# Kernel tuning notes

Hardware: AMD Instinct MI355X
Metric: run time of the kernel (lower is better)

The kernel has to match this reference:

```python
import jax, jax.numpy as jnp
import numpy as np
import math

D_MODEL = 1024
N_HEADS = 16
SEQ = 1024
BATCH = 4


def setup_inputs() -> dict:
    key = jax.random.key(0)
    ks = jax.random.split(key, 13)
    s = 1.0 / math.sqrt(D_MODEL)  # keep logits in a sane range
    return {
        "x": jax.random.normal(ks[0], (BATCH, SEQ, D_MODEL), jnp.float32),
        "Wq": jax.random.normal(ks[1], (D_MODEL, D_MODEL), jnp.float32) * s,
        "bq": jnp.zeros((D_MODEL,), jnp.float32),
        "Wk": jax.random.normal(ks[2], (D_MODEL, D_MODEL), jnp.float32) * s,
        "bk": jnp.zeros((D_MODEL,), jnp.float32),
        "Wv": jax.random.normal(ks[3], (D_MODEL, D_MODEL), jnp.float32) * s,
        "bv": jnp.zeros((D_MODEL,), jnp.float32),
        "Wo": jax.random.normal(ks[4], (D_MODEL, D_MODEL), jnp.float32) * s,
        "bo": jnp.zeros((D_MODEL,), jnp.float32),
        "Wimp": jax.random.normal(ks[5], (N_HEADS, D_MODEL), jnp.float32) * s,
        "bimp": jnp.zeros((N_HEADS,), jnp.float32),
        "k_ema": jax.random.normal(ks[6], (SEQ, D_MODEL), jnp.float32),
        "v_ema": jax.random.normal(ks[7], (SEQ, D_MODEL), jnp.float32),
    }


def reference(x, Wq, bq, Wk, bk, Wv, bv, Wo, bo, Wimp, bimp, k_ema, v_ema):
    B, S, D = x.shape
    H = Wimp.shape[0]
    hd = D // H

    def proj(W, b):
        # [B,S,D] -> [B,H,S,hd]
        return (x @ W.T + b).reshape(B, S, H, hd).transpose(0, 2, 1, 3)

    q = proj(Wq, bq)
    k = proj(Wk, bk)
    v = proj(Wv, bv)

    scores = jnp.einsum("bhqd,bhkd->bhqk", q, k) / math.sqrt(hd)

    # importance bias: outer-sum of per-head key/value importance vectors
    k_imp = (k_ema[:S] @ Wimp.T + bimp).T  # [H, S]
    v_imp = (v_ema[:S] @ Wimp.T + bimp).T  # [H, S]
    bias = 0.5 * (k_imp[:, :, None] + v_imp[:, None, :])  # [H, S, S]
    scores = scores + 0.1 * bias[None]

    # causal mask (torch masks before bias add; -inf + finite == -inf, so equivalent)
    causal = jnp.triu(jnp.ones((S, S), bool), k=1)
    scores = jnp.where(causal, -jnp.inf, scores)

    attn = jax.nn.softmax(scores, axis=-1)
    out = jnp.einsum("bhqk,bhkd->bhqd", attn, v)
    out = out.transpose(0, 2, 1, 3).reshape(B, S, D)
    return out @ Wo.T + bo
```

## Files before the change

### kernel.cpp

```cpp
#include <hip/hip_runtime.h>
#include <hip/hip_bf16.h>
#include <math.h>

#define D_MODEL 1024
#define SEQ     1024
#define BATCH   4
#define NHEADS  16
#define HD      64

#define QSC 0.18033688f
#define BSC 0.072134752f

typedef __bf16 bf16x8 __attribute__((ext_vector_type(8)));
typedef __bf16 bf16x4 __attribute__((ext_vector_type(4)));
typedef float  f32x4  __attribute__((ext_vector_type(4)));

__device__ __forceinline__ f32x4 mfma16(bf16x8 a, bf16x8 b, f32x4 c) {
  return __builtin_amdgcn_mfma_f32_16x16x32_bf16(a, b, c, 0, 0, 0);
}

__device__ __forceinline__ void async16(__bf16* lds, const __bf16* g) {
  __builtin_amdgcn_global_load_lds(g, lds, 16, 0, 0);
}

__global__ __launch_bounds__(256) void prep_kernel(
    const float* __restrict__ x,
    const float* __restrict__ Wq, const float* __restrict__ Wk,
    const float* __restrict__ Wv, const float* __restrict__ Wo,
    const float* __restrict__ v_ema,
    const float* __restrict__ Wimp, const float* __restrict__ bimp,
    __bf16* __restrict__ x_bf, __bf16* __restrict__ wq_bf, __bf16* __restrict__ wk_bf,
    __bf16* __restrict__ wv_bf, __bf16* __restrict__ wo_bf,
    float* __restrict__ vimp) {
  const int bid = blockIdx.x;
  const int tid = threadIdx.x;
  if (bid < 4096) {
    int i = bid * 256 + tid;
    float4 v = ((const float4*)x)[i];
    bf16x4 o; o[0] = (__bf16)v.x; o[1] = (__bf16)v.y; o[2] = (__bf16)v.z; o[3] = (__bf16)v.w;
    ((bf16x4*)x_bf)[i] = o;
  } else if (bid < 8192) {
    int i = (bid - 4096) * 256 + tid;
    int sel = i >> 18;
    int j = i & 262143;
    const float* s = (sel == 0) ? Wq : (sel == 1) ? Wk : (sel == 2) ? Wv : Wo;
    __bf16* d      = (sel == 0) ? wq_bf : (sel == 1) ? wk_bf : (sel == 2) ? wv_bf : wo_bf;
    float4 v = ((const float4*)s)[j];
    bf16x4 o; o[0] = (__bf16)v.x; o[1] = (__bf16)v.y; o[2] = (__bf16)v.z; o[3] = (__bf16)v.w;
    ((bf16x4*)d)[j] = o;
  } else {
    int gw   = (bid - 8192) * 4 + (tid >> 6);
    int lane = tid & 63;
    int h = gw >> 10, s = gw & 1023;
    float sum = 0.f;
    for (int d = lane; d < D_MODEL; d += 64)
      sum += v_ema[s * D_MODEL + d] * Wimp[h * D_MODEL + d];
    for (int mm = 32; mm >= 1; mm >>= 1) sum += __shfl_xor(sum, mm);
    if (lane == 0) vimp[h * SEQ + s] = sum + bimp[h];
  }
}

template<bool OUT_BF16>
__global__ __launch_bounds__(256) void gemm_bt(
    const __bf16* __restrict__ A,
    const __bf16* __restrict__ W0, const __bf16* __restrict__ W1, const __bf16* __restrict__ W2,
    const float* __restrict__ b0, const float* __restrict__ b1, const float* __restrict__ b2,
    void* out0, void* out1, void* out2, float sc0, float sc1, float sc2) {
  const int z = blockIdx.z;
  const __bf16* W   = (z == 0) ? W0 : (z == 1) ? W1 : W2;
  const float* bias = (z == 0) ? b0 : (z == 1) ? b1 : b2;
  void* out         = (z == 0) ? out0 : (z == 1) ? out1 : out2;
  const float sc    = (z == 0) ? sc0 : (z == 1) ? sc1 : sc2;

  __shared__ __bf16 As[128 * 32];
  __shared__ __bf16 Bs[128 * 32];

  const int tid = threadIdx.x;
  const int w = tid >> 6, l = tid & 63;
  const int quad = l >> 4, l16 = l & 15;
  const int wy = w >> 1, wx = w & 1;
  const int row0 = blockIdx.y * 128;
  const int col0 = blockIdx.x * 128;

  const f32x4 fzero = {0.f, 0.f, 0.f, 0.f};
  f32x4 acc[4][4];
  for (int i = 0; i < 4; i++)
    for (int j = 0; j < 4; j++) acc[i][j] = fzero;

  const int lr = l >> 2;
  const int sw0 = (((l & 3) ^ (lr & 3)) * 8);
  const int rowA = w * 16 + lr;
  const __bf16* aptr = A + (size_t)(row0 + rowA) * D_MODEL + sw0;
  const __bf16* bptr = W + (size_t)(col0 + rowA) * D_MODEL + sw0;
  __bf16* lA0 = &As[w * 512 + l * 8];
  __bf16* lA1 = &As[2048 + w * 512 + l * 8];
  __bf16* lB0 = &Bs[w * 512 + l * 8];
  __bf16* lB1 = &Bs[2048 + w * 512 + l * 8];

  const int rswz = (quad ^ (l16 & 3)) * 8;

  for (int k0 = 0; k0 < D_MODEL; k0 += 32) {
    async16(lA0, aptr + k0);
    async16(lA1, aptr + (size_t)64 * D_MODEL + k0);
    async16(lB0, bptr + k0);
    async16(lB1, bptr + (size_t)64 * D_MODEL + k0);
    __syncthreads();
    bf16x8 af[4], bfr[4];
    #pragma unroll
    for (int mi = 0; mi < 4; mi++) af[mi]  = *(const bf16x8*)&As[(wy * 64 + mi * 16 + l16) * 32 + rswz];
    #pragma unroll
    for (int ni = 0; ni < 4; ni++) bfr[ni] = *(const bf16x8*)&Bs[(wx * 64 + ni * 16 + l16) * 32 + rswz];
    if (z == 1) {
      #pragma unroll
      for (int mi = 0; mi < 4; mi++)
        #pragma unroll
        for (int ni = 0; ni < 4; ni++)
          acc[mi][ni] = mfma16(bfr[ni], af[mi], acc[mi][ni]);
    } else {
      #pragma unroll
      for (int mi = 0; mi < 4; mi++)
        #pragma unroll
        for (int ni = 0; ni < 4; ni++)
          acc[mi][ni] = mfma16(af[mi], bfr[ni], acc[mi][ni]);
    }
    __syncthreads();
  }

  if (z == 1 && OUT_BF16) {
    __bf16* kp = (__bf16*)out;
    #pragma unroll
    for (int ni = 0; ni < 4; ni++) {
      const int wcolbase = col0 + wx * 64 + ni * 16 + quad * 4;
      const float4 b4 = *(const float4*)&bias[wcolbase];
      const float bb[4] = {b4.x, b4.y, b4.z, b4.w};
      #pragma unroll
      for (int mi = 0; mi < 4; mi++) {
        const int token = row0 + wy * 64 + mi * 16 + l16;
        const int bh = (token >> 10) * 16 + (wcolbase >> 6);
        const int colp = ((wcolbase & 63) + ((token & 7) << 3)) & 63;
        union { __bf16 hh[4]; uint2 uu; } pk;
        #pragma unroll
        for (int r = 0; r < 4; r++) pk.hh[r] = (__bf16)(acc[mi][ni][r] + bb[r]);
        *(uint2*)(kp + ((size_t)bh * SEQ + (token & 1023)) * HD + colp) = pk.uu;
      }
    }
  } else if (z == 2 && OUT_BF16) {
    __bf16* vp = (__bf16*)out;
    #pragma unroll
    for (int ni = 0; ni < 4; ni++) {
      const int col = col0 + wx * 64 + ni * 16 + l16;
      const float bv = bias[col];
      #pragma unroll
      for (int mi = 0; mi < 4; mi++) {
        const int token = row0 + wy * 64 + mi * 16 + quad * 4;
        const int bh = (token >> 10) * 16 + (col >> 6);
        const int chk = (token >> 6) & 15;
        const int keyp = ((token & 63) + ((col & 7) << 3)) & 63;
        const size_t base = (((size_t)bh * 16 + chk) * 64 + (col & 63)) * 64 + keyp;
        union { __bf16 hh[4]; uint2 uu; } pk;
        #pragma unroll
        for (int r = 0; r < 4; r++) pk.hh[r] = (__bf16)(acc[mi][ni][r] + bv);
        *(uint2*)(vp + base) = pk.uu;
      }
    }
  } else {
    #pragma unroll
    for (int ni = 0; ni < 4; ni++) {
      const int col = col0 + wx * 64 + ni * 16 + l16;
      const float bv = bias[col];
      #pragma unroll
      for (int mi = 0; mi < 4; mi++) {
        const int row = row0 + wy * 64 + mi * 16 + quad * 4;
        #pragma unroll
        for (int r = 0; r < 4; r++) {
          float v = (acc[mi][ni][r] + bv) * sc;
          if (OUT_BF16) ((__bf16*)out)[(size_t)(row + r) * D_MODEL + col] = (__bf16)v;
          else          ((float*)out)[(size_t)(row + r) * D_MODEL + col] = v;
        }
      }
    }
  }
}

__global__ __launch_bounds__(256, 2) void attn_kernel(
    const __bf16* __restrict__ Qb, const __bf16* __restrict__ Kp,
    const __bf16* __restrict__ Vp, const float* __restrict__ vimp,
    __bf16* __restrict__ Ob) {
  const int id = blockIdx.x;
  const int bh = id & 63;
  const int gg = id >> 6;
  const int b = bh >> 4, h = bh & 15;
  const int tid = threadIdx.x;
  const int wave = tid >> 6, lane = tid & 63;
  const int quad = lane >> 4, l16 = lane & 15;

  __shared__ __bf16 Kl[2][4096];
  __shared__ __bf16 Vl[2][4096];
  __shared__ __bf16 Ps[4][16][72];

  const __bf16* kbase = Kp + (size_t)bh * (SEQ * HD);
  const __bf16* vbase = Vp + (size_t)bh * (SEQ * HD);
  const float* vimpH = vimp + h * SEQ;

  const int rot0 = ((quad + (l16 & 7)) & 7) * 8;
  const int rot1 = ((quad + 4 + (l16 & 7)) & 7) * 8;
  const int frow = l16 * 64;

  #pragma unroll 1
  for (int grp = 0; grp < 2; grp++) {
    const int g = grp ? (15 - gg) : gg;
    const int nch = g + 1;
    const int qrow = g * 64 + wave * 16 + l16;
    const __bf16* qp = Qb + (size_t)(b * SEQ + qrow) * D_MODEL + h * HD;
    bf16x8 qa0 = *(const bf16x8*)(qp + quad * 8);
    bf16x8 qa1 = *(const bf16x8*)(qp + 32 + quad * 8);
    float l_i = 0.f;
    f32x4 o[4];
    #pragma unroll
    for (int td = 0; td < 4; td++) { o[td][0] = 0.f; o[td][1] = 0.f; o[td][2] = 0.f; o[td][3] = 0.f; }

    __syncthreads();
    async16(&Kl[0][tid * 8], kbase + tid * 8);
    async16(&Kl[0][2048 + tid * 8], kbase + 2048 + tid * 8);
    async16(&Vl[0][tid * 8], vbase + tid * 8);
    async16(&Vl[0][2048 + tid * 8], vbase + 2048 + tid * 8);

    for (int ch = 0; ch < nch; ch++) {
      const int buf = ch & 1;
      __syncthreads();
      if (ch + 1 < nch) {
        const __bf16* gk = kbase + (ch + 1) * 4096;
        const __bf16* gv = vbase + (ch + 1) * 4096;
        const int nb = buf ^ 1;
        async16(&Kl[nb][tid * 8], gk + tid * 8);
        async16(&Kl[nb][2048 + tid * 8], gk + 2048 + tid * 8);
        async16(&Vl[nb][tid * 8], gv + tid * 8);
        async16(&Vl[nb][2048 + tid * 8], gv + 2048 + tid * 8);
      }
      const int kc = ch * 64;
      float4 vi[4];
      #pragma unroll
      for (int t = 0; t < 4; t++) vi[t] = *(const float4*)(vimpH + kc + t * 16 + quad * 4);
      bf16x8 kf0[4], kf1[4];
      #pragma unroll
      for (int t = 0; t < 4; t++) {
        kf0[t] = *(const bf16x8*)&Kl[buf][t * 1024 + frow + rot0];
        kf1[t] = *(const bf16x8*)&Kl[buf][t * 1024 + frow + rot1];
      }
      bf16x8 vfr0[4], vfr1[4];
      #pragma unroll
      for (int td = 0; td < 4; td++) {
        vfr0[td] = *(const bf16x8*)&Vl[buf][td * 1024 + frow + rot0];
        vfr1[td] = *(const bf16x8*)&Vl[buf][td * 1024 + frow + rot1];
      }
      const f32x4 fz = {0.f, 0.f, 0.f, 0.f};
      float p[4][4];
      float lsum = 0.f;
      #pragma unroll
      for (int t = 0; t < 4; t++) {
        f32x4 sacc = fz;
        sacc = mfma16(kf0[t], qa0, sacc);
        sacc = mfma16(kf1[t], qa1, sacc);
        const float vib[4] = {vi[t].x, vi[t].y, vi[t].z, vi[t].w};
        #pragma unroll
        for (int r = 0; r < 4; r++) {
          float pp = exp2f(sacc[r] + BSC * vib[r]);
          pp = (kc + t * 16 + quad * 4 + r <= qrow) ? pp : 0.f;
          p[t][r] = pp;
          lsum += pp;
        }
      }
      l_i += lsum;
      #pragma unroll
      for (int t = 0; t < 4; t++) {
        union { __bf16 hh[4]; uint2 uu; } pk;
        #pragma unroll
        for (int r = 0; r < 4; r++) pk.hh[r] = (__bf16)p[t][r];
        *(uint2*)&Ps[wave][l16][t * 16 + quad * 4] = pk.uu;
      }
      bf16x8 pf0 = *(const bf16x8*)&Ps[wave][l16][quad * 8];
      bf16x8 pf1 = *(const bf16x8*)&Ps[wave][l16][32 + quad * 8];
      #pragma unroll
      for (int td = 0; td < 4; td++) {
        o[td] = mfma16(vfr0[td], pf0, o[td]);
        o[td] = mfma16(vfr1[td], pf1, o[td]);
      }
    }

    float L = l_i;
    L += __shfl_xor(L, 16);
    L += __shfl_xor(L, 32);
    const float il = 1.0f / L;
    __bf16* op = Ob + (size_t)(b * SEQ + qrow) * D_MODEL + h * HD;
    #pragma unroll
    for (int td = 0; td < 4; td++) {
      union { __bf16 hh[4]; uint2 uu; } pk;
      #pragma unroll
      for (int r = 0; r < 4; r++) pk.hh[r] = (__bf16)(o[td][r] * il);
      *(uint2*)(op + td * 16 + quad * 4) = pk.uu;
    }
  }
}

extern "C" void kernel_launch(void* const* d_in, const int* in_sizes, int n_in,
                              void* d_out, int out_size, void* d_ws, size_t ws_size,
                              hipStream_t stream) {
  const float* x     = (const float*)d_in[0];
  const float* Wq    = (const float*)d_in[1];
  const float* bq    = (const float*)d_in[2];
  const float* Wk    = (const float*)d_in[3];
  const float* bk    = (const float*)d_in[4];
  const float* Wv    = (const float*)d_in[5];
  const float* bv    = (const float*)d_in[6];
  const float* Wo    = (const float*)d_in[7];
  const float* bo    = (const float*)d_in[8];
  const float* Wimp  = (const float*)d_in[9];
  const float* bimp  = (const float*)d_in[10];
  const float* v_ema = (const float*)d_in[12];
  float* out = (float*)d_out;

  char* ws = (char*)d_ws;
  __bf16* x_bf  = (__bf16*)(ws);
  __bf16* wq_bf = (__bf16*)(ws + (8ull  << 20));
  __bf16* wk_bf = (__bf16*)(ws + (10ull << 20));
  __bf16* wv_bf = (__bf16*)(ws + (12ull << 20));
  __bf16* wo_bf = (__bf16*)(ws + (14ull << 20));
  __bf16* q_bf  = (__bf16*)(ws + (16ull << 20));
  __bf16* kp_bf = (__bf16*)(ws + (24ull << 20));
  __bf16* vp_bf = (__bf16*)(ws + (32ull << 20));
  __bf16* a_bf  = (__bf16*)(ws + (40ull << 20));
  float*  vimp  = (float*)(ws + (48ull << 20));

  prep_kernel<<<12288, 256, 0, stream>>>(
      x, Wq, Wk, Wv, Wo, v_ema, Wimp, bimp,
      x_bf, wq_bf, wk_bf, wv_bf, wo_bf, vimp);

  gemm_bt<true><<<dim3(8, 32, 3), 256, 0, stream>>>(
      x_bf, wq_bf, wk_bf, wv_bf, bq, bk, bv,
      (void*)q_bf, (void*)kp_bf, (void*)vp_bf, QSC, 1.0f, 1.0f);

  attn_kernel<<<dim3(512), 256, 0, stream>>>(
      q_bf, kp_bf, vp_bf, vimp, a_bf);

  gemm_bt<false><<<dim3(8, 32, 1), 256, 0, stream>>>(
      a_bf, wo_bf, wo_bf, wo_bf, bo, bo, bo,
      (void*)out, (void*)out, (void*)out, 1.0f, 1.0f, 1.0f);
}
```

Before: 218.2 us.

## Replace QKV projection GEMM with 256x256-tile, 8-wave ping-pong pipelined kernel

Replaces the generic 128x128-tile QKV GEMM with a dedicated kernel that uses 256x256 tiles, 512 threads (8 waves), a K-step of 64, double-buffered LDS filled by direct global-to-LDS loads, and XOR-swizzled LDS layout. The main loop interleaves four MFMA quadrants with asynchronous loads for later K-tiles, using barriers, priority raising and explicit waitcnts to overlap memory with compute. Block IDs are swizzled across 192 blocks for cache locality. The epilogue must reproduce the K/V layouts the attention kernel expects (K swizzled, V transposed into chunks). The cost is high register and LDS use, and a grid of only 192 blocks, which may leave some CUs idle.

```diff
diff --git a/kernel.cpp b/kernel.cpp
--- a/kernel.cpp
+++ b/kernel.cpp
@@ -60,6 +60,177 @@
   }
 }
 
+
+#define STA(BUF, R0, KT) async16(&As[BUF][(R0) * 64 + tid8], aS + (size_t)(R0) * 1024 + (KT) * 64)
+#define STB(BUF, R0, KT) async16(&Bs[BUF][(R0) * 64 + tid8], bS + (size_t)(R0) * 1024 + (KT) * 64)
+
+#define LOAD_A(MH)                                                                      \
+  _Pragma("unroll") for (int mi = 0; mi < 4; ++mi) {                                    \
+    afr[mi][0] = *(const bf16x8*)&As[buf][aro + (MH) * 4096 + mi * 1024 + ph0];         \
+    afr[mi][1] = *(const bf16x8*)&As[buf][aro + (MH) * 4096 + mi * 1024 + (ph0 ^ 32)];  \
+  }
+#define LOAD_B(BF, NH)                                                                  \
+  _Pragma("unroll") for (int ni = 0; ni < 2; ++ni) {                                    \
+    BF[ni][0] = *(const bf16x8*)&Bs[buf][bro + (NH) * 2048 + ni * 1024 + ph0];          \
+    BF[ni][1] = *(const bf16x8*)&Bs[buf][bro + (NH) * 2048 + ni * 1024 + (ph0 ^ 32)];   \
+  }
+
+#define MFMA_QUAD(MB, NB, BF)                                                           \
+  if (zk) {                                                                             \
+    _Pragma("unroll") for (int mi = 0; mi < 4; ++mi)                                    \
+      _Pragma("unroll") for (int ni = 0; ni < 2; ++ni) {                                \
+        acc[(MB) + mi][(NB) + ni] = mfma16(BF[ni][0], afr[mi][0], acc[(MB) + mi][(NB) + ni]); \
+        acc[(MB) + mi][(NB) + ni] = mfma16(BF[ni][1], afr[mi][1], acc[(MB) + mi][(NB) + ni]); \
+      }                                                                                 \
+  } else {                                                                              \
+    _Pragma("unroll") for (int mi = 0; mi < 4; ++mi)                                    \
+      _Pragma("unroll") for (int ni = 0; ni < 2; ++ni) {                                \
+        acc[(MB) + mi][(NB) + ni] = mfma16(afr[mi][0], BF[ni][0], acc[(MB) + mi][(NB) + ni]); \
+        acc[(MB) + mi][(NB) + ni] = mfma16(afr[mi][1], BF[ni][1], acc[(MB) + mi][(NB) + ni]); \
+      }                                                                                 \
+  }
+
+#define BAR() __builtin_amdgcn_s_barrier()
+#define LGKM0()                                           \
+  {                                                       \
+    asm volatile("s_waitcnt lgkmcnt(0)" ::: "memory");    \
+    __builtin_amdgcn_sched_barrier(0);                    \
+  }
+
+__global__ __launch_bounds__(512, 2) void gemm_qkv_8p(
+    const __bf16* __restrict__ A,
+    const __bf16* __restrict__ W0, const __bf16* __restrict__ W1, const __bf16* __restrict__ W2,
+    const float* __restrict__ b0, const float* __restrict__ b1, const float* __restrict__ b2,
+    __bf16* __restrict__ q_out, __bf16* __restrict__ kp, __bf16* __restrict__ vp,
+    float qsc) {
+  const int id = blockIdx.x;
+  const int swz = (id & 7) * 24 + (id >> 3);
+  const int bx = swz & 3, by = (swz >> 2) & 15, z = swz >> 6;
+  const __bf16* W   = (z == 0) ? W0 : (z == 1) ? W1 : W2;
+  const float* bias = (z == 0) ? b0 : (z == 1) ? b1 : b2;
+  const bool zk = (z == 1);
+
+  __shared__ __bf16 As[2][16384];
+  __shared__ __bf16 Bs[2][16384];
+
+  const int tid = threadIdx.x;
+  const int l = tid & 63, wid = tid >> 6;
+  const int quad = l >> 4, l16 = l & 15;
+  const int wy = wid >> 2, wx = wid & 3;
+  const int row0 = by * 256, col0 = bx * 256;
+
+  const int rk = tid >> 3;
+  const int csw = ((tid & 7) ^ (rk & 7)) * 8;
+  const int tid8 = tid * 8;
+  const __bf16* aS = A + (size_t)(row0 + rk) * 1024 + csw;
+  const __bf16* bS = W + (size_t)(col0 + rk) * 1024 + csw;
+
+  const int ph0 = (quad ^ (l16 & 7)) * 8;
+  const int aro = (wy * 128 + l16) * 64;
+  const int bro = (wx * 64 + l16) * 64;
+
+  const f32x4 fzero = {0.f, 0.f, 0.f, 0.f};
+  f32x4 acc[8][4];
+  #pragma unroll
+  for (int i = 0; i < 8; i++)
+    #pragma unroll
+    for (int j = 0; j < 4; j++) acc[i][j] = fzero;
+
+  STA(0, 0, 0);   STA(0, 128, 0); STA(0, 64, 0);  STA(0, 192, 0);
+  STB(0, 0, 0);   STB(0, 64, 0);  STB(0, 128, 0); STB(0, 192, 0);
+  STA(1, 0, 1);   STA(1, 128, 1);
+  STB(1, 0, 1);   STB(1, 64, 1);
+  STA(1, 64, 1);  STA(1, 192, 1);
+  asm volatile("s_waitcnt vmcnt(6)" ::: "memory");
+  BAR();
+
+  #pragma unroll 2
+  for (int t = 0; t < 16; ++t) {
+    const int buf = t & 1, nb = buf ^ 1;
+    bf16x8 afr[4][2], bfr0[2][2], bfr1[2][2];
+    LOAD_A(0);
+    LOAD_B(bfr0, 0);
+    STB(nb, 128, t + 1); STB(nb, 192, t + 1);
+    BAR(); LGKM0();
+    __builtin_amdgcn_s_setprio(1);
+    MFMA_QUAD(0, 0, bfr0);
+    __builtin_amdgcn_s_setprio(0);
+    BAR();
+    LOAD_B(bfr1, 1);
+    STA(buf, 0, t + 2); STA(buf, 128, t + 2);
+    BAR(); LGKM0();
+    __builtin_amdgcn_s_setprio(1);
+    MFMA_QUAD(0, 2, bfr1);
+    __builtin_amdgcn_s_setprio(0);
+    BAR();
+    LOAD_A(1);
+    STB(buf, 0, t + 2); STB(buf, 64, t + 2);
+    BAR(); LGKM0();
+    __builtin_amdgcn_s_setprio(1);
+    MFMA_QUAD(4, 2, bfr1);
+    __builtin_amdgcn_s_setprio(0);
+    BAR();
+    STA(buf, 64, t + 2); STA(buf, 192, t + 2);
+    BAR();
+    __builtin_amdgcn_s_setprio(1);
+    MFMA_QUAD(4, 0, bfr0);
+    __builtin_amdgcn_s_setprio(0);
+    asm volatile("s_waitcnt vmcnt(6)" ::: "memory");
+    BAR();
+  }
+  asm volatile("s_waitcnt vmcnt(0)" ::: "memory");
+
+  if (z == 1) {
+    #pragma unroll
+    for (int ni = 0; ni < 4; ++ni) {
+      const int wcolbase = col0 + wx * 64 + ni * 16 + quad * 4;
+      const float4 b4 = *(const float4*)&bias[wcolbase];
+      const float bb[4] = {b4.x, b4.y, b4.z, b4.w};
+      #pragma unroll
+      for (int mi = 0; mi < 8; ++mi) {
+        const int token = row0 + wy * 128 + mi * 16 + l16;
+        const int bh = (token >> 10) * 16 + (wcolbase >> 6);
+        const int colp = ((wcolbase & 63) + ((token & 7) << 3)) & 63;
+        union { __bf16 hh[4]; uint2 uu; } pk;
+        #pragma unroll
+        for (int r = 0; r < 4; ++r) pk.hh[r] = (__bf16)(acc[mi][ni][r] + bb[r]);
+        *(uint2*)(kp + ((size_t)bh * SEQ + (token & 1023)) * HD + colp) = pk.uu;
+      }
+    }
+  } else if (z == 2) {
+    #pragma unroll
+    for (int ni = 0; ni < 4; ++ni) {
+      const int col = col0 + wx * 64 + ni * 16 + l16;
+      const float bv = bias[col];
+      #pragma unroll
+      for (int mi = 0; mi < 8; ++mi) {
+        const int token = row0 + wy * 128 + mi * 16 + quad * 4;
+        const int bh = (token >> 10) * 16 + (col >> 6);
+        const int chk = (token >> 6) & 15;
+        const int keyp = ((token & 63) + ((col & 7) << 3)) & 63;
+        const size_t base = (((size_t)bh * 16 + chk) * 64 + (col & 63)) * 64 + keyp;
+        union { __bf16 hh[4]; uint2 uu; } pk;
+        #pragma unroll
+        for (int r = 0; r < 4; ++r) pk.hh[r] = (__bf16)(acc[mi][ni][r] + bv);
+        *(uint2*)(vp + base) = pk.uu;
+      }
+    }
+  } else {
+    #pragma unroll
+    for (int ni = 0; ni < 4; ++ni) {
+      const int col = col0 + wx * 64 + ni * 16 + l16;
+      const float bv = bias[col];
+      #pragma unroll
+      for (int mi = 0; mi < 8; ++mi) {
+        const int row = row0 + wy * 128 + mi * 16 + quad * 4;
+        #pragma unroll
+        for (int r = 0; r < 4; ++r)
+          q_out[(size_t)(row + r) * D_MODEL + col] = (__bf16)((acc[mi][ni][r] + bv) * qsc);
+      }
+    }
+  }
+}
+
 template<bool OUT_BF16>
 __global__ __launch_bounds__(256) void gemm_bt(
     const __bf16* __restrict__ A,
@@ -335,9 +506,9 @@
       x, Wq, Wk, Wv, Wo, v_ema, Wimp, bimp,
       x_bf, wq_bf, wk_bf, wv_bf, wo_bf, vimp);
 
-  gemm_bt<true><<<dim3(8, 32, 3), 256, 0, stream>>>(
+  gemm_qkv_8p<<<192, 512, 0, stream>>>(
       x_bf, wq_bf, wk_bf, wv_bf, bq, bk, bv,
-      (void*)q_bf, (void*)kp_bf, (void*)vp_bf, QSC, 1.0f, 1.0f);
+      q_bf, kp_bf, vp_bf, QSC);
 
   attn_kernel<<<dim3(512), 256, 0, stream>>>(
       q_bf, kp_bf, vp_bf, vimp, a_bf);
```

New measurement: 217.9 us. No clear change (-0.2%).
